# Kernel optimization log

Measured on AMD Instinct MI355X. Metric: run time of the kernel, lower is better.

The kernel has to match this reference:

```python
import jax, jax.numpy as jnp
import numpy as np

EPS = 1e-12

def setup_inputs() -> dict:
    key = jax.random.key(0)
    k1, k2, k3, k4, k5, k6 = jax.random.split(key, 6)
    B, DIM, T = 16, 256, 2048
    K, D = 1024, 64  # num_embeddings, embedding_dim
    N = B * T
    input_data = jax.random.normal(k1, (B, DIM, T), dtype=jnp.float32)
    codebooks = jax.random.normal(k2, (K, D), dtype=jnp.float32)
    W_in = jax.random.normal(k3, (DIM, D), dtype=jnp.float32) / np.sqrt(DIM)
    b_in = jnp.zeros((D,), dtype=jnp.float32)
    W_out = jax.random.normal(k4, (D, DIM), dtype=jnp.float32) / np.sqrt(D)
    b_out = jnp.zeros((DIM,), dtype=jnp.float32)
    random_vector = jax.random.normal(k5, (N, D), dtype=jnp.float32)
    return {"input_data": input_data, "codebooks": codebooks,
            "W_in": W_in, "b_in": b_in, "W_out": W_out, "b_out": b_out,
            "random_vector": random_vector}

def reference(input_data, codebooks, W_in, b_in, W_out, b_out, random_vector):
    B, DIM, T = input_data.shape
    D = codebooks.shape[1]
    # encode: [B, DIM, T] -> [B, T, DIM] -> project -> [B*T, D]
    x = jnp.einsum('bct,cd->btd', input_data, W_in) + b_in
    x = x.reshape(-1, D)  # [N, D]
    distances = (jnp.sum(x * x, axis=1, keepdims=True)
                 - 2.0 * (x @ codebooks.T)
                 + jnp.sum(codebooks * codebooks, axis=1)[None, :])  # [N, K]
    min_indices = jnp.argmin(distances, axis=1)  # [N]
    hard = codebooks[min_indices]  # [N, D]
    # noise substitution
    norm_resid = jnp.sqrt(jnp.sum((x - hard) ** 2, axis=1, keepdims=True))
    norm_rand = jnp.sqrt(jnp.sum(random_vector ** 2, axis=1, keepdims=True))
    vq_error = (norm_resid / (norm_rand + EPS)) * random_vector
    q = x + vq_error  # [N, D]
    # decode: [N, D] -> [B, T, D] -> project_out -> [B, DIM, T]
    q = q.reshape(B, T, D)
    out = jnp.einsum('btd,dc->bct', q, W_out) + b_out[None, :, None]
    return out
```

## Files before the change

### kernel.cpp

```cpp
#include <hip/hip_runtime.h>
#include <hip/hip_bf16.h>

typedef __bf16 bf16x8 __attribute__((ext_vector_type(8)));
typedef unsigned short u16x8 __attribute__((ext_vector_type(8)));
typedef unsigned int u32x2 __attribute__((ext_vector_type(2)));
typedef float f32x4 __attribute__((ext_vector_type(4)));
typedef unsigned short u16;

constexpr int DIMc = 256, Tt = 2048, Dd = 64;

#define CBF_U  0
#define CN_U   65536
#define WINT_U 67584
#define WOX_U  83968

__device__ __forceinline__ u16 f2b(float f) {
  unsigned u = __float_as_uint(f);
  return (u16)((u + 0x7FFFu + ((u >> 16) & 1u)) >> 16);
}
__device__ __forceinline__ float b2f(u16 v) {
  return __uint_as_float(((unsigned)v) << 16);
}
__device__ __forceinline__ unsigned f2b2(float a, float b) {
  return (unsigned)f2b(a) | ((unsigned)f2b(b) << 16);
}
__device__ __forceinline__ f32x4 mfma16(u16x8 a, u16x8 b, f32x4 c) {
  return __builtin_amdgcn_mfma_f32_16x16x32_bf16(
      __builtin_bit_cast(bf16x8, a), __builtin_bit_cast(bf16x8, b), c, 0, 0, 0);
}
__device__ __forceinline__ void dma16(const u16* g, u16* l) {
  __builtin_amdgcn_global_load_lds(
      (const __attribute__((address_space(1))) unsigned int*)g,
      (__attribute__((address_space(3))) unsigned int*)l, 16, 0, 0);
}

__global__ void nsvq_prep(const float* __restrict__ cb, const float* __restrict__ Win,
                          const float* __restrict__ Wout, u16* __restrict__ wsu) {
  const int g = blockIdx.x * 256 + threadIdx.x;
  {
    const int k = g >> 4, j = (g & 15) << 2;
    float4 v = *(const float4*)(cb + k * 64 + j);
    u16* row = wsu + CBF_U + k * 64 + j;
    row[0] = f2b(-2.f * v.x); row[1] = f2b(-2.f * v.y);
    row[2] = f2b(-2.f * v.z); row[3] = f2b(-2.f * v.w);
  }
  if (g < 1024) {
    const float* cr = cb + g * 64;
    float p[4];
    #pragma unroll
    for (int q = 0; q < 4; ++q) {
      float4 a0 = ((const float4*)(cr + q * 8))[0],      a1 = ((const float4*)(cr + q * 8))[1];
      float4 a2 = ((const float4*)(cr + 32 + q * 8))[0], a3 = ((const float4*)(cr + 32 + q * 8))[1];
      float pA = fmaf(a0.w, a0.w, fmaf(a0.z, a0.z, fmaf(a0.y, a0.y, a0.x * a0.x)));
      float pB = fmaf(a1.w, a1.w, fmaf(a1.z, a1.z, fmaf(a1.y, a1.y, a1.x * a1.x)));
      float pC = fmaf(a2.w, a2.w, fmaf(a2.z, a2.z, fmaf(a2.y, a2.y, a2.x * a2.x)));
      float pD = fmaf(a3.w, a3.w, fmaf(a3.z, a3.z, fmaf(a3.y, a3.y, a3.x * a3.x)));
      p[q] = (pA + pB) + (pC + pD);
    }
    ((float*)(wsu + CN_U))[g] = (p[0] + p[1]) + (p[2] + p[3]);
  }
  {
    const int d = g >> 8, c = g & 255;
    wsu[WINT_U + d * 256 + (((c >> 3) ^ (d & 7)) << 3) + (c & 7)] = f2b(Win[c * 64 + d]);
  }
  {
    const int c = g >> 6, d = g & 63;
    wsu[WOX_U + c * 64 + (((d >> 3) ^ (c & 7)) << 3) + (d & 7)] = f2b(Wout[d * 256 + c]);
  }
}

__global__ __launch_bounds__(256, 3) void nsvq_main(
    const float* __restrict__ in, const float* __restrict__ rnd,
    const float* __restrict__ bin, const float* __restrict__ bout,
    const u16* __restrict__ wsu, float* __restrict__ out) {
  __shared__ u16 sm[20992];
  u16* const WinT = sm;
  u16* const WoX  = sm;
  u16* const Xt   = sm + 16384;
  float* const mnp = (float*)(sm + 20480);

  const int tid  = threadIdx.x;
  const int lane = tid & 63;
  const int w    = tid >> 6;
  const int quad = lane >> 4, col = lane & 15;
  const int b    = blockIdx.x >> 5;
  const int t0   = (blockIdx.x & 31) << 6;
  const int myt  = w * 16 + col;

  #pragma unroll
  for (int ii = 0; ii < 8; ++ii) {
    const int i = w + 4 * ii;
    dma16(wsu + WINT_U + i * 512 + lane * 8, WinT + i * 512);
  }
  u16x8 Bf[8];
  const float* ibase = in + (size_t)b * DIMc * Tt + t0 + myt;
  #pragma unroll
  for (int kt = 0; kt < 8; ++kt) {
    float v[8];
    #pragma unroll
    for (int j = 0; j < 8; ++j) v[j] = ibase[(size_t)(kt * 32 + quad * 8 + j) * Tt];
    u16x8 pk;
    #pragma unroll
    for (int j = 0; j < 8; ++j) pk[j] = f2b(v[j]);
    Bf[kt] = pk;
  }
  float rr2v = 0.f, rv[16];
  const float* rb = rnd + ((size_t)b * Tt + t0) * Dd;
  #pragma unroll
  for (int tt = 0; tt < 16; ++tt) {
    rv[tt] = rb[(size_t)(w * 16 + tt) * Dd + lane];
    float s = rv[tt] * rv[tt];
    s += __shfl_xor(s, 1);  s += __shfl_xor(s, 2);  s += __shfl_xor(s, 4);
    s += __shfl_xor(s, 8);  s += __shfl_xor(s, 16); s += __shfl_xor(s, 32);
    if (col == tt) rr2v = s;
  }
  __syncthreads();

  f32x4 acc[4];
  #pragma unroll
  for (int mt = 0; mt < 4; ++mt) {
    float4 bi = *(const float4*)(bin + mt * 16 + quad * 4);
    f32x4 a = {bi.x, bi.y, bi.z, bi.w};
    const int d = mt * 16 + col;
    #pragma unroll
    for (int kt = 0; kt < 8; ++kt) {
      u16x8 A = *(const u16x8*)(WinT + d * 256 + (((kt * 4 + quad) ^ (d & 7)) << 3));
      a = mfma16(A, Bf[kt], a);
    }
    acc[mt] = a;
  }
  float x2v = 0.f;
  #pragma unroll
  for (int mt = 0; mt < 4; ++mt) {
    #pragma unroll
    for (int r = 0; r < 4; ++r) x2v = fmaf(acc[mt][r], acc[mt][r], x2v);
    u32x2 px = { f2b2(acc[mt][0], acc[mt][1]), f2b2(acc[mt][2], acc[mt][3]) };
    const int bk  = mt * 2 + (quad >> 1);
    const int off = myt * 64 + ((bk ^ (myt & 7)) << 3) + (quad & 1) * 4;
    *(u32x2*)(Xt + off) = px;
  }
  x2v += __shfl_xor(x2v, 16);
  x2v += __shfl_xor(x2v, 32);
  __syncthreads();

  #pragma unroll
  for (int ii = 0; ii < 8; ++ii) {
    const int i = w + 4 * ii;
    dma16(wsu + WOX_U + i * 512 + lane * 8, WoX + i * 512);
  }
  u16x8 Xa[4], Xb[4];
  #pragma unroll
  for (int nt = 0; nt < 4; ++nt) {
    const int tr = nt * 16 + col;
    Xa[nt] = *(const u16x8*)(Xt + tr * 64 + ((quad ^ (tr & 7)) << 3));
    Xb[nt] = *(const u16x8*)(Xt + tr * 64 + (((4 + quad) ^ (tr & 7)) << 3));
  }
  float minv[4];
  #pragma unroll
  for (int i = 0; i < 4; ++i) minv[i] = 3.4e38f;
  const u16* cwf   = wsu + CBF_U + (size_t)(w * 256) * 64;
  const float* cnp = (const float*)(wsu + CN_U) + w * 256;
  #pragma unroll 4
  for (int mi = 0; mi < 16; ++mi) {
    u16x8 A0 = *(const u16x8*)(cwf + (mi * 16 + col) * 64 + quad * 8);
    u16x8 A1 = *(const u16x8*)(cwf + (mi * 16 + col) * 64 + 32 + quad * 8);
    f32x4 cn4 = *(const f32x4*)(cnp + mi * 16 + quad * 4);
    #pragma unroll
    for (int nt = 0; nt < 4; ++nt) {
      f32x4 a = mfma16(A0, Xa[nt], cn4);
      a = mfma16(A1, Xb[nt], a);
      #pragma unroll
      for (int r = 0; r < 4; ++r) minv[nt] = fminf(minv[nt], a[r]);
    }
  }
  #pragma unroll
  for (int nt = 0; nt < 4; ++nt) {
    float m = minv[nt];
    m = fminf(m, __shfl_xor(m, 16));
    m = fminf(m, __shfl_xor(m, 32));
    mnp[w * 64 + nt * 16 + col] = m;
  }
  __syncthreads();

  float mv = 3.4e38f;
  #pragma unroll
  for (int j = 0; j < 4; ++j) mv = fminf(mv, mnp[j * 64 + myt]);
  float r2  = fmaxf(x2v + mv, 0.f);
  float scv = sqrtf(r2) / (sqrtf(rr2v) + 1e-12f);
  #pragma unroll
  for (int tt = 0; tt < 16; ++tt) {
    float s  = __shfl(scv, tt);
    const int tr  = w * 16 + tt;
    const int idx = tr * 64 + (((lane >> 3) ^ (tr & 7)) << 3) + (lane & 7);
    Xt[idx] = f2b(fmaf(s, rv[tt], b2f(Xt[idx])));
  }

  u16x8 Q0 = *(const u16x8*)(Xt + myt * 64 + ((quad ^ (myt & 7)) << 3));
  u16x8 Q1 = *(const u16x8*)(Xt + myt * 64 + (((4 + quad) ^ (myt & 7)) << 3));
  float* ob0 = out + (size_t)b * DIMc * Tt + t0 + myt;
  #pragma unroll
  for (int mt = 0; mt < 16; ++mt) {
    const int c = mt * 16 + col;
    const u16* ar = WoX + c * 64;
    u16x8 A0 = *(const u16x8*)(ar + ((quad ^ (c & 7)) << 3));
    u16x8 A1 = *(const u16x8*)(ar + (((4 + quad) ^ (c & 7)) << 3));
    float4 bo = *(const float4*)(bout + mt * 16 + quad * 4);
    f32x4 a = {bo.x, bo.y, bo.z, bo.w};
    a = mfma16(A0, Q0, a);
    a = mfma16(A1, Q1, a);
    float* ob = ob0 + (size_t)(mt * 16 + quad * 4) * Tt;
    #pragma unroll
    for (int r = 0; r < 4; ++r) ob[(size_t)r * Tt] = a[r];
  }
}

extern "C" void kernel_launch(void* const* d_in, const int* in_sizes, int n_in,
                              void* d_out, int out_size, void* d_ws, size_t ws_size,
                              hipStream_t stream) {
  const float *in = nullptr, *cbp = nullptr, *rnd = nullptr, *bin = nullptr, *bout = nullptr;
  const float* w16[2] = {nullptr, nullptr}; int nw = 0;
  for (int i = 0; i < n_in; ++i) {
    switch (in_sizes[i]) {
      case 8388608: in  = (const float*)d_in[i]; break;
      case 65536:   cbp = (const float*)d_in[i]; break;
      case 2097152: rnd = (const float*)d_in[i]; break;
      case 64:      bin = (const float*)d_in[i]; break;
      case 256:     bout= (const float*)d_in[i]; break;
      case 16384:   if (nw < 2) w16[nw++] = (const float*)d_in[i]; break;
      default: break;
    }
  }
  if (!in)   in  = (const float*)d_in[0];
  if (!cbp)  cbp = (const float*)d_in[1];
  if (nw < 2) { w16[0] = (const float*)d_in[2]; w16[1] = (const float*)d_in[4]; }
  if (!bin)  bin = (const float*)d_in[3];
  if (!bout) bout = (const float*)d_in[5];
  if (!rnd)  rnd = (const float*)d_in[6];

  u16* wsu = (u16*)d_ws;
  nsvq_prep<<<64, 256, 0, stream>>>(cbp, w16[0], w16[1], wsu);
  nsvq_main<<<512, 256, 0, stream>>>(in, rnd, bin, bout, wsu, (float*)d_out);
}
```

Baseline: 115.8 us.

## Prefetch W_out early, load noise in MFMA layout, fuse noise add in registers

Gives W_out its own shared-memory region so its DMA can be issued at kernel start and overlap the input loads and encoder, instead of waiting until after the encode barrier. Random vectors are now read as float4 in the same per-lane layout as the MFMA accumulator. This replaces the 16-step shuffle reduction with a local sum plus two shuffles. The noise is added directly to the fp32 accumulators before packing to bf16, which removes a shared-memory read-modify-write and one bf16 rounding of x. The cost is roughly 75KB of shared memory per block, so launch bounds drop from 3 to 2 blocks per SM, lowering occupancy.

```diff
diff --git a/kernel.cpp b/kernel.cpp
--- a/kernel.cpp
+++ b/kernel.cpp
@@ -69,15 +69,15 @@
   }
 }
 
-__global__ __launch_bounds__(256, 3) void nsvq_main(
+__global__ __launch_bounds__(256, 2) void nsvq_main(
     const float* __restrict__ in, const float* __restrict__ rnd,
     const float* __restrict__ bin, const float* __restrict__ bout,
     const u16* __restrict__ wsu, float* __restrict__ out) {
-  __shared__ u16 sm[20992];
+  __shared__ u16 sm[37376];
   u16* const WinT = sm;
-  u16* const WoX  = sm;
-  u16* const Xt   = sm + 16384;
-  float* const mnp = (float*)(sm + 20480);
+  u16* const WoX  = sm + 16384;
+  u16* const Xt   = sm + 32768;
+  float* const mnp = (float*)(sm + 36864);
 
   const int tid  = threadIdx.x;
   const int lane = tid & 63;
@@ -92,6 +92,11 @@
     const int i = w + 4 * ii;
     dma16(wsu + WINT_U + i * 512 + lane * 8, WinT + i * 512);
   }
+  #pragma unroll
+  for (int ii = 0; ii < 8; ++ii) {
+    const int i = w + 4 * ii;
+    dma16(wsu + WOX_U + i * 512 + lane * 8, WoX + i * 512);
+  }
   u16x8 Bf[8];
   const float* ibase = in + (size_t)b * DIMc * Tt + t0 + myt;
   #pragma unroll
@@ -104,16 +109,20 @@
     for (int j = 0; j < 8; ++j) pk[j] = f2b(v[j]);
     Bf[kt] = pk;
   }
-  float rr2v = 0.f, rv[16];
-  const float* rb = rnd + ((size_t)b * Tt + t0) * Dd;
-  #pragma unroll
-  for (int tt = 0; tt < 16; ++tt) {
-    rv[tt] = rb[(size_t)(w * 16 + tt) * Dd + lane];
-    float s = rv[tt] * rv[tt];
-    s += __shfl_xor(s, 1);  s += __shfl_xor(s, 2);  s += __shfl_xor(s, 4);
-    s += __shfl_xor(s, 8);  s += __shfl_xor(s, 16); s += __shfl_xor(s, 32);
-    if (col == tt) rr2v = s;
-  }
+  float4 rq[4];
+  {
+    const float* rbase = rnd + ((size_t)b * Tt + t0 + myt) * Dd + quad * 4;
+    #pragma unroll
+    for (int mt = 0; mt < 4; ++mt) rq[mt] = *(const float4*)(rbase + mt * 16);
+  }
+  float rr2v = 0.f;
+  #pragma unroll
+  for (int mt = 0; mt < 4; ++mt) {
+    rr2v = fmaf(rq[mt].x, rq[mt].x, rr2v); rr2v = fmaf(rq[mt].y, rq[mt].y, rr2v);
+    rr2v = fmaf(rq[mt].z, rq[mt].z, rr2v); rr2v = fmaf(rq[mt].w, rq[mt].w, rr2v);
+  }
+  rr2v += __shfl_xor(rr2v, 16);
+  rr2v += __shfl_xor(rr2v, 32);
   __syncthreads();
 
   f32x4 acc[4];
@@ -143,11 +152,6 @@
   x2v += __shfl_xor(x2v, 32);
   __syncthreads();
 
-  #pragma unroll
-  for (int ii = 0; ii < 8; ++ii) {
-    const int i = w + 4 * ii;
-    dma16(wsu + WOX_U + i * 512 + lane * 8, WoX + i * 512);
-  }
   u16x8 Xa[4], Xb[4];
   #pragma unroll
   for (int nt = 0; nt < 4; ++nt) {
@@ -188,11 +192,15 @@
   float r2  = fmaxf(x2v + mv, 0.f);
   float scv = sqrtf(r2) / (sqrtf(rr2v) + 1e-12f);
   #pragma unroll
-  for (int tt = 0; tt < 16; ++tt) {
-    float s  = __shfl(scv, tt);
-    const int tr  = w * 16 + tt;
-    const int idx = tr * 64 + (((lane >> 3) ^ (tr & 7)) << 3) + (lane & 7);
-    Xt[idx] = f2b(fmaf(s, rv[tt], b2f(Xt[idx])));
+  for (int mt = 0; mt < 4; ++mt) {
+    float q0 = fmaf(scv, rq[mt].x, acc[mt][0]);
+    float q1 = fmaf(scv, rq[mt].y, acc[mt][1]);
+    float q2 = fmaf(scv, rq[mt].z, acc[mt][2]);
+    float q3 = fmaf(scv, rq[mt].w, acc[mt][3]);
+    u32x2 pq = { f2b2(q0, q1), f2b2(q2, q3) };
+    const int bk  = mt * 2 + (quad >> 1);
+    const int off = myt * 64 + ((bk ^ (myt & 7)) << 3) + (quad & 1) * 4;
+    *(u32x2*)(Xt + off) = pq;
   }
 
   u16x8 Q0 = *(const u16x8*)(Xt + myt * 64 + ((quad ^ (myt & 7)) << 3));
```

New measurement: 113.0 us. -2.4%, faster.

## Halve per-block token tile and split projections across wave pairs

Applied to the files above, without the earlier changes.

Each block now handles 32 tokens instead of 64, doubling the grid to 1024 blocks. Waves are paired so each pair splits the input projection's D rows and the output projection's channel rows, with partial norms combined through shared memory. The noise vector is loaded per thread in the MFMA accumulator layout and added to the fp32 projection result directly, rather than read back from bf16 shared memory. The aim is more blocks and higher occupancy (launch bounds 4) to hide memory latency. The cost is that every codebook sweep is now amortised over half as many tokens, doubling global codebook reads, plus an extra barrier.

```diff
diff --git a/kernel.cpp b/kernel.cpp
--- a/kernel.cpp
+++ b/kernel.cpp
@@ -17,9 +17,6 @@
 __device__ __forceinline__ u16 f2b(float f) {
   unsigned u = __float_as_uint(f);
   return (u16)((u + 0x7FFFu + ((u >> 16) & 1u)) >> 16);
-}
-__device__ __forceinline__ float b2f(u16 v) {
-  return __uint_as_float(((unsigned)v) << 16);
 }
 __device__ __forceinline__ unsigned f2b2(float a, float b) {
   return (unsigned)f2b(a) | ((unsigned)f2b(b) << 16);
@@ -69,23 +66,24 @@
   }
 }
 
-__global__ __launch_bounds__(256, 3) void nsvq_main(
+__global__ __launch_bounds__(256, 4) void nsvq_main(
     const float* __restrict__ in, const float* __restrict__ rnd,
     const float* __restrict__ bin, const float* __restrict__ bout,
     const u16* __restrict__ wsu, float* __restrict__ out) {
-  __shared__ u16 sm[20992];
+  __shared__ u16 sm[18944];
   u16* const WinT = sm;
   u16* const WoX  = sm;
   u16* const Xt   = sm + 16384;
-  float* const mnp = (float*)(sm + 20480);
+  float* const fz = (float*)(sm + 18432);
 
   const int tid  = threadIdx.x;
   const int lane = tid & 63;
   const int w    = tid >> 6;
+  const int th   = w >> 1, mh = w & 1;
   const int quad = lane >> 4, col = lane & 15;
-  const int b    = blockIdx.x >> 5;
-  const int t0   = (blockIdx.x & 31) << 6;
-  const int myt  = w * 16 + col;
+  const int b    = blockIdx.x >> 6;
+  const int t0   = (blockIdx.x & 63) << 5;
+  const int myt  = th * 16 + col;
 
   #pragma unroll
   for (int ii = 0; ii < 8; ++ii) {
@@ -104,21 +102,23 @@
     for (int j = 0; j < 8; ++j) pk[j] = f2b(v[j]);
     Bf[kt] = pk;
   }
-  float rr2v = 0.f, rv[16];
-  const float* rb = rnd + ((size_t)b * Tt + t0) * Dd;
-  #pragma unroll
-  for (int tt = 0; tt < 16; ++tt) {
-    rv[tt] = rb[(size_t)(w * 16 + tt) * Dd + lane];
-    float s = rv[tt] * rv[tt];
-    s += __shfl_xor(s, 1);  s += __shfl_xor(s, 2);  s += __shfl_xor(s, 4);
-    s += __shfl_xor(s, 8);  s += __shfl_xor(s, 16); s += __shfl_xor(s, 32);
-    if (col == tt) rr2v = s;
-  }
-  __syncthreads();
-
-  f32x4 acc[4];
-  #pragma unroll
-  for (int mt = 0; mt < 4; ++mt) {
+  const float* rbase = rnd + ((size_t)b * Tt + t0 + myt) * Dd + mh * 32 + quad * 4;
+  float4 rq0 = *(const float4*)(rbase);
+  float4 rq1 = *(const float4*)(rbase + 16);
+  float rr2p = 0.f;
+  rr2p = fmaf(rq0.x, rq0.x, rr2p); rr2p = fmaf(rq0.y, rq0.y, rr2p);
+  rr2p = fmaf(rq0.z, rq0.z, rr2p); rr2p = fmaf(rq0.w, rq0.w, rr2p);
+  rr2p = fmaf(rq1.x, rq1.x, rr2p); rr2p = fmaf(rq1.y, rq1.y, rr2p);
+  rr2p = fmaf(rq1.z, rq1.z, rr2p); rr2p = fmaf(rq1.w, rq1.w, rr2p);
+  rr2p += __shfl_xor(rr2p, 16);
+  rr2p += __shfl_xor(rr2p, 32);
+  if (quad == 0) fz[192 + mh * 32 + myt] = rr2p;
+  __syncthreads();
+
+  f32x4 acc[2];
+  #pragma unroll
+  for (int mi = 0; mi < 2; ++mi) {
+    const int mt = mh * 2 + mi;
     float4 bi = *(const float4*)(bin + mt * 16 + quad * 4);
     f32x4 a = {bi.x, bi.y, bi.z, bi.w};
     const int d = mt * 16 + col;
@@ -127,20 +127,22 @@
       u16x8 A = *(const u16x8*)(WinT + d * 256 + (((kt * 4 + quad) ^ (d & 7)) << 3));
       a = mfma16(A, Bf[kt], a);
     }
-    acc[mt] = a;
-  }
-  float x2v = 0.f;
-  #pragma unroll
-  for (int mt = 0; mt < 4; ++mt) {
-    #pragma unroll
-    for (int r = 0; r < 4; ++r) x2v = fmaf(acc[mt][r], acc[mt][r], x2v);
-    u32x2 px = { f2b2(acc[mt][0], acc[mt][1]), f2b2(acc[mt][2], acc[mt][3]) };
+    acc[mi] = a;
+  }
+  float x2p = 0.f;
+  #pragma unroll
+  for (int mi = 0; mi < 2; ++mi) {
+    const int mt = mh * 2 + mi;
+    #pragma unroll
+    for (int r = 0; r < 4; ++r) x2p = fmaf(acc[mi][r], acc[mi][r], x2p);
+    u32x2 px = { f2b2(acc[mi][0], acc[mi][1]), f2b2(acc[mi][2], acc[mi][3]) };
     const int bk  = mt * 2 + (quad >> 1);
     const int off = myt * 64 + ((bk ^ (myt & 7)) << 3) + (quad & 1) * 4;
     *(u32x2*)(Xt + off) = px;
   }
-  x2v += __shfl_xor(x2v, 16);
-  x2v += __shfl_xor(x2v, 32);
+  x2p += __shfl_xor(x2p, 16);
+  x2p += __shfl_xor(x2p, 32);
+  if (quad == 0) fz[128 + mh * 32 + myt] = x2p;
   __syncthreads();
 
   #pragma unroll
@@ -148,16 +150,14 @@
     const int i = w + 4 * ii;
     dma16(wsu + WOX_U + i * 512 + lane * 8, WoX + i * 512);
   }
-  u16x8 Xa[4], Xb[4];
-  #pragma unroll
-  for (int nt = 0; nt < 4; ++nt) {
+  u16x8 Xa[2], Xb[2];
+  #pragma unroll
+  for (int nt = 0; nt < 2; ++nt) {
     const int tr = nt * 16 + col;
     Xa[nt] = *(const u16x8*)(Xt + tr * 64 + ((quad ^ (tr & 7)) << 3));
     Xb[nt] = *(const u16x8*)(Xt + tr * 64 + (((4 + quad) ^ (tr & 7)) << 3));
   }
-  float minv[4];
-  #pragma unroll
-  for (int i = 0; i < 4; ++i) minv[i] = 3.4e38f;
+  float minv[2] = {3.4e38f, 3.4e38f};
   const u16* cwf   = wsu + CBF_U + (size_t)(w * 256) * 64;
   const float* cnp = (const float*)(wsu + CN_U) + w * 256;
   #pragma unroll 4
@@ -166,7 +166,7 @@
     u16x8 A1 = *(const u16x8*)(cwf + (mi * 16 + col) * 64 + 32 + quad * 8);
     f32x4 cn4 = *(const f32x4*)(cnp + mi * 16 + quad * 4);
     #pragma unroll
-    for (int nt = 0; nt < 4; ++nt) {
+    for (int nt = 0; nt < 2; ++nt) {
       f32x4 a = mfma16(A0, Xa[nt], cn4);
       a = mfma16(A1, Xb[nt], a);
       #pragma unroll
@@ -174,32 +174,40 @@
     }
   }
   #pragma unroll
-  for (int nt = 0; nt < 4; ++nt) {
+  for (int nt = 0; nt < 2; ++nt) {
     float m = minv[nt];
     m = fminf(m, __shfl_xor(m, 16));
     m = fminf(m, __shfl_xor(m, 32));
-    mnp[w * 64 + nt * 16 + col] = m;
-  }
-  __syncthreads();
-
-  float mv = 3.4e38f;
-  #pragma unroll
-  for (int j = 0; j < 4; ++j) mv = fminf(mv, mnp[j * 64 + myt]);
+    if (quad == 0) fz[w * 32 + nt * 16 + col] = m;
+  }
+  __syncthreads();
+
+  float mv = fminf(fminf(fz[myt], fz[32 + myt]), fminf(fz[64 + myt], fz[96 + myt]));
+  float x2v  = fz[128 + myt] + fz[160 + myt];
+  float rr2v = fz[192 + myt] + fz[224 + myt];
   float r2  = fmaxf(x2v + mv, 0.f);
   float scv = sqrtf(r2) / (sqrtf(rr2v) + 1e-12f);
   #pragma unroll
-  for (int tt = 0; tt < 16; ++tt) {
-    float s  = __shfl(scv, tt);
-    const int tr  = w * 16 + tt;
-    const int idx = tr * 64 + (((lane >> 3) ^ (tr & 7)) << 3) + (lane & 7);
-    Xt[idx] = f2b(fmaf(s, rv[tt], b2f(Xt[idx])));
-  }
+  for (int mi = 0; mi < 2; ++mi) {
+    const int mt = mh * 2 + mi;
+    float4 r = mi ? rq1 : rq0;
+    float q0 = fmaf(scv, r.x, acc[mi][0]);
+    float q1 = fmaf(scv, r.y, acc[mi][1]);
+    float q2 = fmaf(scv, r.z, acc[mi][2]);
+    float q3 = fmaf(scv, r.w, acc[mi][3]);
+    u32x2 pq = { f2b2(q0, q1), f2b2(q2, q3) };
+    const int bk  = mt * 2 + (quad >> 1);
+    const int off = myt * 64 + ((bk ^ (myt & 7)) << 3) + (quad & 1) * 4;
+    *(u32x2*)(Xt + off) = pq;
+  }
+  __syncthreads();
 
   u16x8 Q0 = *(const u16x8*)(Xt + myt * 64 + ((quad ^ (myt & 7)) << 3));
   u16x8 Q1 = *(const u16x8*)(Xt + myt * 64 + (((4 + quad) ^ (myt & 7)) << 3));
   float* ob0 = out + (size_t)b * DIMc * Tt + t0 + myt;
   #pragma unroll
-  for (int mt = 0; mt < 16; ++mt) {
+  for (int mi = 0; mi < 8; ++mi) {
+    const int mt = mh * 8 + mi;
     const int c = mt * 16 + col;
     const u16* ar = WoX + c * 64;
     u16x8 A0 = *(const u16x8*)(ar + ((quad ^ (c & 7)) << 3));
@@ -239,5 +247,5 @@
 
   u16* wsu = (u16*)d_ws;
   nsvq_prep<<<64, 256, 0, stream>>>(cbp, w16[0], w16[1], wsu);
-  nsvq_main<<<512, 256, 0, stream>>>(in, rnd, bin, bout, wsu, (float*)d_out);
-}
+  nsvq_main<<<1024, 256, 0, stream>>>(in, rnd, bin, bout, wsu, (float*)d_out);
+}
```

New measurement: 124.1 us. 7.2% more time.
